# Kernel optimization log

Measured on AMD Instinct MI355X. Metric: run time of the kernel, lower is better.

Reference implementation:

```python
import jax, jax.numpy as jnp
import numpy as np

N, T, C = 100000, 12, 32  # nodes, periods, hidden (A3TGCN out_channels hardcoded 32)
E = 3_200_000


def setup_inputs() -> dict:
    key = jax.random.key(0)
    ks = jax.random.split(key, 20)
    s_g = 1.0 / np.sqrt(1.0)        # GCNConv glorot-ish for in=1
    s_l = 1.0 / np.sqrt(2.0 * C)    # torch Linear default for in=2C
    s_h = 1.0 / np.sqrt(C)
    u = lambda k, shape, s: jax.random.uniform(k, shape, jnp.float32, -s, s)
    return {
        "x": jax.random.normal(ks[0], (N, T), jnp.float32),
        "edge_index": jax.random.randint(ks[1], (2, E), 0, N, jnp.int32),
        "edge_weight": jax.random.uniform(ks[2], (E,), jnp.float32),
        # TGCN gate GCNConv params (in_channels=1, out=C)
        "w_z": u(ks[3], (1, C), s_g), "b_z": jnp.zeros((C,), jnp.float32),
        "w_r": u(ks[4], (1, C), s_g), "b_r": jnp.zeros((C,), jnp.float32),
        "w_h": u(ks[5], (1, C), s_g), "b_h": jnp.zeros((C,), jnp.float32),
        # TGCN gate Linear params (torch layout [out=C, in=2C])
        "lw_z": u(ks[6], (C, 2 * C), s_l), "lb_z": u(ks[7], (C,), s_l),
        "lw_r": u(ks[8], (C, 2 * C), s_l), "lb_r": u(ks[9], (C,), s_l),
        "lw_h": u(ks[10], (C, 2 * C), s_l), "lb_h": u(ks[11], (C,), s_l),
        # A3TGCN temporal attention
        "att": jax.random.uniform(ks[12], (T,), jnp.float32),
        # head Linear(32, 1)
        "head_w": u(ks[13], (1, C), s_h), "head_b": u(ks[14], (1,), s_h),
    }


def reference(x, edge_index, edge_weight, w_z, b_z, w_r, b_r, w_h, b_h,
              lw_z, lb_z, lw_r, lb_r, lw_h, lb_h, att, head_w, head_b):
    n = x.shape[0]
    # --- GCN normalization with self-loops (fill value 1) ---
    loop = jnp.arange(n)
    s = jnp.concatenate([edge_index[0], loop])
    d = jnp.concatenate([edge_index[1], loop])
    w = jnp.concatenate([edge_weight, jnp.ones((n,), edge_weight.dtype)])
    deg = jax.ops.segment_sum(w, d, num_segments=n)
    dinv = jnp.where(deg > 0, jax.lax.rsqrt(deg), 0.0)
    norm = dinv[s] * w * dinv[d]
    # --- shared sparse aggregation: A_hat @ X for all periods at once ---
    # in_channels = 1, so GCNConv(X_t) = (A_hat x_t) * W + b; aggregate scalars [N,T]
    agg = jax.ops.segment_sum(norm[:, None] * x[s], d, num_segments=n)  # [N, T]
    # gate convolutions, [N, T, C]
    cz = agg[:, :, None] * w_z[0] + b_z
    ch = agg[:, :, None] * w_h[0] + b_h
    # A3TGCN passes H=None every period -> hidden starts at 0 each step, so
    # linear([conv, H]) reduces to conv @ W[:, :C].T + b, and the reset gate R
    # multiplies H=0 (no effect on output).
    Z = jax.nn.sigmoid(jnp.einsum('ntc,oc->nto', cz, lw_z[:, :C]) + lb_z)
    Ht = jnp.tanh(jnp.einsum('ntc,oc->nto', ch, lw_h[:, :C]) + lb_h)
    Hp = (1.0 - Z) * Ht  # per-period hidden state, [N, T, C]
    probs = jax.nn.softmax(att)
    h = jnp.einsum('t,ntc->nc', probs, Hp)  # attention-weighted temporal sum
    h = jax.nn.relu(h)
    return h @ head_w.T + head_b  # [N, 1]
```

## Files before the change

kernel.cpp:

```cpp
#include <hip/hip_runtime.h>

#define N_NODES 100000
#define T_P 12
#define C_H 32
#define E_EDGES 3200000

#define NODES_PER_B 128
#define NB 782
#define MAX_BE 4608

#define VEC_E (E_EDGES / 4)
#define P1_THREADS 512
#define P1_VECS 2048
#define NBLK1 ((VEC_E + P1_VECS - 1) / P1_VECS)


__global__ void params_kernel(const float* __restrict__ wz, const float* __restrict__ bz,
                              const float* __restrict__ wh, const float* __restrict__ bh,
                              const float* __restrict__ lwz, const float* __restrict__ lbz,
                              const float* __restrict__ lwh, const float* __restrict__ lbh,
                              const float* __restrict__ att, float* __restrict__ P,
                              int* __restrict__ cursor) {
    int o = threadIdx.x;
    if (o < NB) cursor[o] = 0;
    if (o < C_H) {
        float az = 0.f, bzv = 0.f, ah = 0.f, bhv = 0.f;
        for (int c = 0; c < C_H; ++c) {
            float lz = lwz[o * 2 * C_H + c];
            float lh = lwh[o * 2 * C_H + c];
            az += wz[c] * lz;  bzv += bz[c] * lz;
            ah += wh[c] * lh;  bhv += bh[c] * lh;
        }
        P[16 + o]  = az;  P[48 + o]  = bzv + lbz[o];
        P[80 + o]  = ah;  P[112 + o] = bhv + lbh[o];
    }
    if (o == 0) {
        float m = -1e30f;
        for (int t = 0; t < T_P; ++t) m = fmaxf(m, att[t]);
        float e[T_P], s = 0.f;
        for (int t = 0; t < T_P; ++t) { e[t] = __expf(att[t] - m); s += e[t]; }
        float inv = 1.0f / s;
        for (int t = 0; t < T_P; ++t) P[t] = e[t] * inv;
    }
}

__global__ void bucket_scatter_kernel(const int* __restrict__ src, const int* __restrict__ dst,
                                      const float* __restrict__ w, int* __restrict__ cursor,
                                      float2* __restrict__ entries) {
    __shared__ int h[NB];
    __shared__ int claim[NB];
    for (int i = threadIdx.x; i < NB; i += P1_THREADS) h[i] = 0;
    __syncthreads();
    const int4* d4 = (const int4*)dst;
    int vbase = blockIdx.x * P1_VECS;
    int4 dc[4];
    int4 rk[4];
#pragma unroll
    for (int k = 0; k < 4; ++k) {
        int v = vbase + threadIdx.x + k * P1_THREADS;
        if (v < VEC_E) {
            int4 d = d4[v];
            dc[k] = d;
            rk[k].x = atomicAdd(&h[d.x >> 7], 1);
            rk[k].y = atomicAdd(&h[d.y >> 7], 1);
            rk[k].z = atomicAdd(&h[d.z >> 7], 1);
            rk[k].w = atomicAdd(&h[d.w >> 7], 1);
        }
    }
    __syncthreads();
    for (int i = threadIdx.x; i < NB; i += P1_THREADS) {
        int c = h[i];
        claim[i] = c ? atomicAdd(&cursor[i], c) : 0;
    }
    __syncthreads();
    const int4* s4 = (const int4*)src;
    const float4* w4 = (const float4*)w;
#pragma unroll
    for (int k = 0; k < 4; ++k) {
        int v = vbase + threadIdx.x + k * P1_THREADS;
        if (v < VEC_E) {
            int4 s = s4[v];
            float4 ww = w4[v];
            int4 d = dc[k];
            int bin, dl, pos;
            bin = d.x >> 7; dl = d.x & 127;
            pos = claim[bin] + rk[k].x;
            if (pos < MAX_BE) entries[bin * MAX_BE + pos] = make_float2(__int_as_float(s.x | (dl << 17)), ww.x);
            bin = d.y >> 7; dl = d.y & 127;
            pos = claim[bin] + rk[k].y;
            if (pos < MAX_BE) entries[bin * MAX_BE + pos] = make_float2(__int_as_float(s.y | (dl << 17)), ww.y);
            bin = d.z >> 7; dl = d.z & 127;
            pos = claim[bin] + rk[k].z;
            if (pos < MAX_BE) entries[bin * MAX_BE + pos] = make_float2(__int_as_float(s.z | (dl << 17)), ww.z);
            bin = d.w >> 7; dl = d.w & 127;
            pos = claim[bin] + rk[k].w;
            if (pos < MAX_BE) entries[bin * MAX_BE + pos] = make_float2(__int_as_float(s.w | (dl << 17)), ww.w);
        }
    }
}

__global__ void __launch_bounds__(512)
degree_kernel(const float2* __restrict__ entries, const int* __restrict__ cursor,
              float* __restrict__ dinv) {
    __shared__ float wsum[NODES_PER_B];
    int tid = threadIdx.x;
    int b = blockIdx.x;
    int lo = b * MAX_BE;
    int ne = cursor[b]; if (ne > MAX_BE) ne = MAX_BE;
    if (tid < NODES_PER_B) wsum[tid] = 0.f;
    __syncthreads();
    for (int k = tid; k < ne; k += 512) {
        float2 e = entries[lo + k];
        atomicAdd(&wsum[(__float_as_int(e.x) >> 17) & 127], e.y);
    }
    __syncthreads();
    if (tid < NODES_PER_B) {
        int n = (b << 7) + tid;
        if (n < N_NODES) dinv[n] = rsqrtf(1.0f + wsum[tid]);
    }
}

__global__ void y_kernel(const float* __restrict__ x, const float* __restrict__ dinv,
                         float* __restrict__ y) {
    int n = blockIdx.x * blockDim.x + threadIdx.x;
    if (n >= N_NODES) return;
    float din = dinv[n];
    const float4* xn = (const float4*)(x + (size_t)n * T_P);
    float4 a0 = xn[0], a1 = xn[1], a2 = xn[2];
    a0.x *= din; a0.y *= din; a0.z *= din; a0.w *= din;
    a1.x *= din; a1.y *= din; a1.z *= din; a1.w *= din;
    a2.x *= din; a2.y *= din; a2.z *= din; a2.w *= din;
    float4* yn = (float4*)(y + ((size_t)n << 4));
    yn[0] = a0; yn[1] = a1; yn[2] = a2;
    yn[3] = make_float4(0.f, 0.f, 0.f, 0.f);
}

__global__ void __launch_bounds__(512)
sort_gather_kernel(const float2* __restrict__ entries, const int* __restrict__ cursor,
                   const float* __restrict__ dinv, const float* __restrict__ y,
                   const float* __restrict__ P, const float* __restrict__ head_w,
                   const float* __restrict__ head_b, float* __restrict__ out) {
    __shared__ float2 stage[MAX_BE];
    __shared__ unsigned short sidx[MAX_BE];
    __shared__ int   cnt[NODES_PER_B];
    __shared__ int   inc[NODES_PER_B];
    __shared__ int   rnk[NODES_PER_B];
    __shared__ float Ps[160];
    __shared__ float hws[C_H];
    int tid = threadIdx.x;
    int b = blockIdx.x;
    int lo = b * MAX_BE;
    int ne = cursor[b]; if (ne > MAX_BE) ne = MAX_BE;
    if (tid < 160) Ps[tid] = P[tid];
    if (tid < C_H) hws[tid] = head_w[tid];
    if (tid < NODES_PER_B) cnt[tid] = 0;
    __syncthreads();
    for (int k = tid; k < ne; k += 512) {
        float2 e = entries[lo + k];
        stage[k] = e;
        atomicAdd(&cnt[(__float_as_int(e.x) >> 17) & 127], 1);
    }
    __syncthreads();
    if (tid < NODES_PER_B) inc[tid] = cnt[tid];
    __syncthreads();
    for (int d = 1; d < NODES_PER_B; d <<= 1) {
        int t = (tid >= d && tid < NODES_PER_B) ? inc[tid - d] : 0;
        __syncthreads();
        if (tid < NODES_PER_B) inc[tid] += t;
        __syncthreads();
    }
    if (tid < NODES_PER_B) rnk[tid] = inc[tid] - cnt[tid];
    __syncthreads();
    for (int k = tid; k < ne; k += 512) {
        int dl = (__float_as_int(stage[k].x) >> 17) & 127;
        int r = atomicAdd(&rnk[dl], 1);
        sidx[r] = (unsigned short)k;
    }
    __syncthreads();
    int nl = tid >> 2, lane = tid & 3;
    int n = (b << 7) + nl;
    if (n >= N_NODES) return;
    int end = inc[nl];
    int start = end - cnt[nl];
    const float4* yn = (const float4*)(y + ((size_t)n << 4));
    float4 a0 = make_float4(0.f, 0.f, 0.f, 0.f);
    float4 a1 = a0, a2 = a0;
    if (lane == 0)      a0 = yn[0];
    else if (lane == 1) a1 = yn[1];
    else if (lane == 2) a2 = yn[2];
    for (int j = start + lane; j < end; j += 4) {
        float2 ent = stage[sidx[j]];
        int s = __float_as_int(ent.x) & 0x1FFFF;
        float c = ent.y;
        const float4* ys = (const float4*)(y + ((size_t)s << 4));
        float4 s0 = ys[0], s1 = ys[1], s2 = ys[2];
        a0.x += c * s0.x; a0.y += c * s0.y; a0.z += c * s0.z; a0.w += c * s0.w;
        a1.x += c * s1.x; a1.y += c * s1.y; a1.z += c * s1.z; a1.w += c * s1.w;
        a2.x += c * s2.x; a2.y += c * s2.y; a2.z += c * s2.z; a2.w += c * s2.w;
    }
#define RED4(v) v += __shfl_xor(v, 1); v += __shfl_xor(v, 2)
    RED4(a0.x); RED4(a0.y); RED4(a0.z); RED4(a0.w);
    RED4(a1.x); RED4(a1.y); RED4(a1.z); RED4(a1.w);
    RED4(a2.x); RED4(a2.y); RED4(a2.z); RED4(a2.w);
#undef RED4
    float din = dinv[n];
    float av[T_P];
    av[0] = a0.x * din; av[1] = a0.y * din; av[2]  = a0.z * din; av[3]  = a0.w * din;
    av[4] = a1.x * din; av[5] = a1.y * din; av[6]  = a1.z * din; av[7]  = a1.w * din;
    av[8] = a2.x * din; av[9] = a2.y * din; av[10] = a2.z * din; av[11] = a2.w * din;
    float acc = 0.f;
#pragma unroll
    for (int k = 0; k < 8; ++k) {
        int c = (lane << 3) + k;
        float Az = Ps[16 + c], Bz = Ps[48 + c], Ah = Ps[80 + c], Bh = Ps[112 + c];
        float hc = 0.f;
#pragma unroll
        for (int t = 0; t < T_P; ++t) {
            float a = av[t];
            float oz = 1.f / (1.f + __expf(a * Az + Bz));
            float vv = a * Ah + Bh;
            float th = 1.f - 2.f / (1.f + __expf(2.f * vv));
            hc += Ps[t] * oz * th;
        }
        acc += fmaxf(hc, 0.f) * hws[c];
    }
    acc += __shfl_xor(acc, 1);
    acc += __shfl_xor(acc, 2);
    if (lane == 0) out[n] = acc + head_b[0];
}

extern "C" void kernel_launch(void* const* d_in, const int* in_sizes, int n_in,
                              void* d_out, int out_size, void* d_ws, size_t ws_size,
                              hipStream_t stream) {
    const float* x    = (const float*)d_in[0];
    const int*   ei   = (const int*)d_in[1];
    const float* ew   = (const float*)d_in[2];
    const float* w_z  = (const float*)d_in[3];
    const float* b_z  = (const float*)d_in[4];
    const float* w_h  = (const float*)d_in[7];
    const float* b_h  = (const float*)d_in[8];
    const float* lw_z = (const float*)d_in[9];
    const float* lb_z = (const float*)d_in[10];
    const float* lw_h = (const float*)d_in[13];
    const float* lb_h = (const float*)d_in[14];
    const float* att  = (const float*)d_in[15];
    const float* hw   = (const float*)d_in[16];
    const float* hb   = (const float*)d_in[17];
    float* out = (float*)d_out;

    float* wsf      = (float*)d_ws;
    float* P        = wsf;
    float* dinv     = P + 256;
    int*   cursor   = (int*)(dinv + N_NODES);
    float* y        = wsf + 101040;
    float2* entries = (float2*)(y + (size_t)N_NODES * 16);

    const int* srcp = ei;
    const int* dstp = ei + E_EDGES;

    params_kernel<<<1, 1024, 0, stream>>>(w_z, b_z, w_h, b_h, lw_z, lb_z, lw_h, lb_h,
                                          att, P, cursor);
    bucket_scatter_kernel<<<NBLK1, P1_THREADS, 0, stream>>>(srcp, dstp, ew, cursor, entries);
    degree_kernel<<<NB, 512, 0, stream>>>(entries, cursor, dinv);
    y_kernel<<<(N_NODES + 255) / 256, 256, 0, stream>>>(x, dinv, y);
    sort_gather_kernel<<<NB, 512, 0, stream>>>(entries, cursor, dinv, y, P, hw, hb, out);
}
```

Baseline: 253.6 us.

## Locally sort edges by bucket in shared memory before scatter; fuse degree and y kernels

Result: faster. 243.4 us (-4.0%).

```diff
diff --git a/kernel.cpp b/kernel.cpp
--- a/kernel.cpp
+++ b/kernel.cpp
@@ -11,7 +11,8 @@
 
 #define VEC_E (E_EDGES / 4)
 #define P1_THREADS 512
-#define P1_VECS 2048
+#define P1_VECS 1024
+#define EPB 4096
 #define NBLK1 ((VEC_E + P1_VECS - 1) / P1_VECS)
 
 
@@ -44,67 +45,101 @@
     }
 }
 
-__global__ void bucket_scatter_kernel(const int* __restrict__ src, const int* __restrict__ dst,
-                                      const float* __restrict__ w, int* __restrict__ cursor,
-                                      float2* __restrict__ entries) {
+__global__ void __launch_bounds__(512)
+bucket_scatter_kernel(const int* __restrict__ src, const int* __restrict__ dst,
+                      const float* __restrict__ w, int* __restrict__ cursor,
+                      float2* __restrict__ entries) {
+    __shared__ float2 stage[EPB];
+    __shared__ unsigned short bina[EPB];
+    __shared__ unsigned short sidx[EPB];
     __shared__ int h[NB];
+    __shared__ int scanb[1024];
     __shared__ int claim[NB];
-    for (int i = threadIdx.x; i < NB; i += P1_THREADS) h[i] = 0;
+    int tid = threadIdx.x;
+    int vbase = blockIdx.x * P1_VECS;
+    int ne = E_EDGES - vbase * 4;
+    if (ne > EPB) ne = EPB;
+    for (int i = tid; i < NB; i += 512) h[i] = 0;
     __syncthreads();
     const int4* d4 = (const int4*)dst;
-    int vbase = blockIdx.x * P1_VECS;
-    int4 dc[4];
-    int4 rk[4];
-#pragma unroll
-    for (int k = 0; k < 4; ++k) {
-        int v = vbase + threadIdx.x + k * P1_THREADS;
-        if (v < VEC_E) {
+    const int4* s4 = (const int4*)src;
+    const float4* w4 = (const float4*)w;
+    int rra[8];
+    int valid[2];
+#pragma unroll
+    for (int half = 0; half < 2; ++half) {
+        int v = vbase + half * 512 + tid;
+        valid[half] = (v < VEC_E);
+        if (valid[half]) {
             int4 d = d4[v];
-            dc[k] = d;
-            rk[k].x = atomicAdd(&h[d.x >> 7], 1);
-            rk[k].y = atomicAdd(&h[d.y >> 7], 1);
-            rk[k].z = atomicAdd(&h[d.z >> 7], 1);
-            rk[k].w = atomicAdd(&h[d.w >> 7], 1);
-        }
-    }
-    __syncthreads();
-    for (int i = threadIdx.x; i < NB; i += P1_THREADS) {
+            int4 s = s4[v];
+            float4 ww = w4[v];
+            int kb = half * 2048 + tid;
+            int bin, dl;
+            bin = d.x >> 7; dl = d.x & 127;
+            rra[half * 4 + 0] = atomicAdd(&h[bin], 1);
+            stage[kb] = make_float2(__int_as_float(s.x | (dl << 17)), ww.x);
+            bina[kb] = (unsigned short)bin;
+            bin = d.y >> 7; dl = d.y & 127;
+            rra[half * 4 + 1] = atomicAdd(&h[bin], 1);
+            stage[kb + 512] = make_float2(__int_as_float(s.y | (dl << 17)), ww.y);
+            bina[kb + 512] = (unsigned short)bin;
+            bin = d.z >> 7; dl = d.z & 127;
+            rra[half * 4 + 2] = atomicAdd(&h[bin], 1);
+            stage[kb + 1024] = make_float2(__int_as_float(s.z | (dl << 17)), ww.z);
+            bina[kb + 1024] = (unsigned short)bin;
+            bin = d.w >> 7; dl = d.w & 127;
+            rra[half * 4 + 3] = atomicAdd(&h[bin], 1);
+            stage[kb + 1536] = make_float2(__int_as_float(s.w | (dl << 17)), ww.w);
+            bina[kb + 1536] = (unsigned short)bin;
+        }
+    }
+    __syncthreads();
+    scanb[tid]       = (tid < NB) ? h[tid] : 0;
+    scanb[tid + 512] = (tid + 512 < NB) ? h[tid + 512] : 0;
+    __syncthreads();
+    for (int d = 1; d < 1024; d <<= 1) {
+        int t0 = (tid >= d) ? scanb[tid - d] : 0;
+        int t1 = (tid + 512 >= d) ? scanb[tid + 512 - d] : 0;
+        __syncthreads();
+        scanb[tid] += t0;
+        scanb[tid + 512] += t1;
+        __syncthreads();
+    }
+    for (int i = tid; i < NB; i += 512) {
         int c = h[i];
         claim[i] = c ? atomicAdd(&cursor[i], c) : 0;
     }
-    __syncthreads();
-    const int4* s4 = (const int4*)src;
-    const float4* w4 = (const float4*)w;
-#pragma unroll
-    for (int k = 0; k < 4; ++k) {
-        int v = vbase + threadIdx.x + k * P1_THREADS;
-        if (v < VEC_E) {
-            int4 s = s4[v];
-            float4 ww = w4[v];
-            int4 d = dc[k];
-            int bin, dl, pos;
-            bin = d.x >> 7; dl = d.x & 127;
-            pos = claim[bin] + rk[k].x;
-            if (pos < MAX_BE) entries[bin * MAX_BE + pos] = make_float2(__int_as_float(s.x | (dl << 17)), ww.x);
-            bin = d.y >> 7; dl = d.y & 127;
-            pos = claim[bin] + rk[k].y;
-            if (pos < MAX_BE) entries[bin * MAX_BE + pos] = make_float2(__int_as_float(s.y | (dl << 17)), ww.y);
-            bin = d.z >> 7; dl = d.z & 127;
-            pos = claim[bin] + rk[k].z;
-            if (pos < MAX_BE) entries[bin * MAX_BE + pos] = make_float2(__int_as_float(s.z | (dl << 17)), ww.z);
-            bin = d.w >> 7; dl = d.w & 127;
-            pos = claim[bin] + rk[k].w;
-            if (pos < MAX_BE) entries[bin * MAX_BE + pos] = make_float2(__int_as_float(s.w | (dl << 17)), ww.w);
-        }
+#pragma unroll
+    for (int half = 0; half < 2; ++half) {
+        if (valid[half]) {
+            int kb = half * 2048 + tid;
+#pragma unroll
+            for (int j = 0; j < 4; ++j) {
+                int k = kb + j * 512;
+                int b = bina[k];
+                sidx[scanb[b] - h[b] + rra[half * 4 + j]] = (unsigned short)k;
+            }
+        }
+    }
+    __syncthreads();
+    for (int p = tid; p < ne; p += 512) {
+        int k = sidx[p];
+        float2 e = stage[k];
+        int b = bina[k];
+        int pos = claim[b] + (p - (scanb[b] - h[b]));
+        if (pos < MAX_BE) entries[b * MAX_BE + pos] = e;
     }
 }
 
 __global__ void __launch_bounds__(512)
-degree_kernel(const float2* __restrict__ entries, const int* __restrict__ cursor,
-              float* __restrict__ dinv) {
+prep_kernel(const float2* __restrict__ entries, const int* __restrict__ cursor,
+            const float* __restrict__ x, float* __restrict__ dinv, float* __restrict__ y) {
     __shared__ float wsum[NODES_PER_B];
+    __shared__ float dloc[NODES_PER_B];
     int tid = threadIdx.x;
     int b = blockIdx.x;
+    int nbase = b << 7;
     int lo = b * MAX_BE;
     int ne = cursor[b]; if (ne > MAX_BE) ne = MAX_BE;
     if (tid < NODES_PER_B) wsum[tid] = 0.f;
@@ -115,24 +150,26 @@
     }
     __syncthreads();
     if (tid < NODES_PER_B) {
-        int n = (b << 7) + tid;
-        if (n < N_NODES) dinv[n] = rsqrtf(1.0f + wsum[tid]);
-    }
-}
-
-__global__ void y_kernel(const float* __restrict__ x, const float* __restrict__ dinv,
-                         float* __restrict__ y) {
-    int n = blockIdx.x * blockDim.x + threadIdx.x;
-    if (n >= N_NODES) return;
-    float din = dinv[n];
-    const float4* xn = (const float4*)(x + (size_t)n * T_P);
-    float4 a0 = xn[0], a1 = xn[1], a2 = xn[2];
-    a0.x *= din; a0.y *= din; a0.z *= din; a0.w *= din;
-    a1.x *= din; a1.y *= din; a1.z *= din; a1.w *= din;
-    a2.x *= din; a2.y *= din; a2.z *= din; a2.w *= din;
-    float4* yn = (float4*)(y + ((size_t)n << 4));
-    yn[0] = a0; yn[1] = a1; yn[2] = a2;
-    yn[3] = make_float4(0.f, 0.f, 0.f, 0.f);
+        int n = nbase + tid;
+        float di = (n < N_NODES) ? rsqrtf(1.0f + wsum[tid]) : 0.f;
+        dloc[tid] = di;
+        if (n < N_NODES) dinv[n] = di;
+    }
+    __syncthreads();
+    if (tid < 384) {
+        int nl = tid / 3, q = tid - nl * 3;
+        int n = nbase + nl;
+        if (n < N_NODES) {
+            float4 v = ((const float4*)x)[(size_t)n * 3 + q];
+            float di = dloc[nl];
+            v.x *= di; v.y *= di; v.z *= di; v.w *= di;
+            ((float4*)y)[((size_t)n << 2) + q] = v;
+        }
+    }
+    if (tid < NODES_PER_B) {
+        int n = nbase + tid;
+        if (n < N_NODES) ((float4*)y)[((size_t)n << 2) + 3] = make_float4(0.f, 0.f, 0.f, 0.f);
+    }
 }
 
 __global__ void __launch_bounds__(512)
@@ -261,7 +298,6 @@
     params_kernel<<<1, 1024, 0, stream>>>(w_z, b_z, w_h, b_h, lw_z, lb_z, lw_h, lb_h,
                                           att, P, cursor);
     bucket_scatter_kernel<<<NBLK1, P1_THREADS, 0, stream>>>(srcp, dstp, ew, cursor, entries);
-    degree_kernel<<<NB, 512, 0, stream>>>(entries, cursor, dinv);
-    y_kernel<<<(N_NODES + 255) / 256, 256, 0, stream>>>(x, dinv, y);
+    prep_kernel<<<NB, 512, 0, stream>>>(entries, cursor, x, dinv, y);
     sort_gather_kernel<<<NB, 512, 0, stream>>>(entries, cursor, dinv, y, P, hw, hb, out);
 }
```
